# Kernel optimization log

Hardware: AMD Instinct MI355X
Metric: run time of the kernel (lower is better)

Reference implementation:

```python
import jax, jax.numpy as jnp
import numpy as np

TOP_K = 2  # num_experts_per_tok


def setup_inputs() -> dict:
    key = jax.random.key(0)
    k1, k2, k3, k4, k5 = jax.random.split(key, 5)
    T, H, F, E = 2048, 2048, 1024, 8
    hidden_states = jax.random.normal(k1, (T, H), dtype=jnp.float32)
    router_logits = jax.random.normal(k2, (T, E), dtype=jnp.float32)
    s = 1.0 / np.sqrt(H)
    w1 = jax.random.normal(k3, (E, H, F), dtype=jnp.float32) * s  # gate proj
    w3 = jax.random.normal(k4, (E, H, F), dtype=jnp.float32) * s  # up proj
    w2 = jax.random.normal(k5, (E, F, H), dtype=jnp.float32) * (1.0 / np.sqrt(F))  # down proj
    return {"hidden_states": hidden_states, "router_logits": router_logits,
            "w1": w1, "w3": w3, "w2": w2}


def reference(hidden_states, router_logits, w1, w3, w2):
    # Top-K routing: softmax over raw logits, take top-k probs as combine weights
    # (renormalize_topk_logits=False, routed_scaling_factor=None).
    T, E = router_logits.shape
    probs = jax.nn.softmax(router_logits.astype(jnp.float32), axis=-1)  # (T, E)
    topk_w, topk_ids = jax.lax.top_k(probs, TOP_K)                      # (T, K)
    # Scatter combine weights into a dense (T, E) matrix (zeros off top-k).
    combine = jnp.zeros((T, E), dtype=probs.dtype).at[
        jnp.arange(T)[:, None], topk_ids].add(topk_w)                    # (T, E)

    x = hidden_states
    # SwiGLU expert FFN computed per-expert (dense over all tokens, masked by
    # combine weights -> same math as fused dispatch/grouped-GEMM/combine).
    g = jnp.einsum('th,ehf->etf', x, w1)          # (E, T, F) gate
    u = jnp.einsum('th,ehf->etf', x, w3)          # (E, T, F) up
    act = jax.nn.silu(g) * u                      # (E, T, F)
    act = act * combine.T[:, :, None]             # apply combine weight pre-down-proj
    y = jnp.einsum('etf,efh->th', act, w2)        # (T, H) combined over experts
    return y.astype(hidden_states.dtype)
```

## Files before the change

### kernel.cpp

```cpp
#include <hip/hip_runtime.h>
#include <stdint.h>

#define T_TOK 2048
#define HDIM  2048
#define FDIM  1024
#define NEXP  8

#define BM   128
#define BN   64
#define BK   64
#define NTHR 256
#define MT_MAX 16
#define NT1 (FDIM / BN)
#define NT2 (HDIM / BN)
#define NK1 (HDIM / BK)
#define NK2 (FDIM / BK)
#define GRID1 (NEXP * MT_MAX * NT1)
#define GRID2 (NEXP * MT_MAX * NT2)

typedef unsigned short u16;
typedef __attribute__((ext_vector_type(16))) float f32x16;
typedef __attribute__((ext_vector_type(8))) short bf16x8;

__device__ __forceinline__ u16 f2bf(float f) {
  uint32_t u = __float_as_uint(f);
  u += 0x7FFFu + ((u >> 16) & 1u);
  return (u16)(u >> 16);
}

__device__ __forceinline__ void glds16(const u16* src, u16* dst) {
  __builtin_amdgcn_global_load_lds(
      (const __attribute__((address_space(1))) uint32_t*)src,
      (__attribute__((address_space(3))) uint32_t*)dst, 16, 0, 0);
}

__global__ void route1_kernel(const float* __restrict__ logits,
                              int* __restrict__ tok_e, float* __restrict__ tok_w,
                              int* __restrict__ counts) {
  __shared__ int lcnt[NEXP];
  const int tid = threadIdx.x;
  const int t = blockIdx.x * 256 + tid;
  if (tid < NEXP) lcnt[tid] = 0;
  __syncthreads();
  float l[NEXP];
#pragma unroll
  for (int e = 0; e < NEXP; ++e) l[e] = logits[t * NEXP + e];
  float m = l[0];
#pragma unroll
  for (int e = 1; e < NEXP; ++e) m = fmaxf(m, l[e]);
  float p[NEXP]; float s = 0.f;
#pragma unroll
  for (int e = 0; e < NEXP; ++e) { p[e] = __expf(l[e] - m); s += p[e]; }
  float inv = 1.f / s;
  int i0 = 0; float p0 = p[0];
#pragma unroll
  for (int e = 1; e < NEXP; ++e) if (p[e] > p0) { p0 = p[e]; i0 = e; }
  int i1 = -1; float p1 = -1.f;
#pragma unroll
  for (int e = 0; e < NEXP; ++e) if (e != i0 && p[e] > p1) { p1 = p[e]; i1 = e; }
  tok_e[t] = i0 | (i1 << 8);
  tok_w[t * 2]     = p0 * inv;
  tok_w[t * 2 + 1] = p1 * inv;
  atomicAdd(&lcnt[i0], 1);
  atomicAdd(&lcnt[i1], 1);
  __syncthreads();
  if (tid < NEXP) atomicAdd(&counts[tid], lcnt[tid]);
}

__global__ void route2_kernel(const int* __restrict__ counts,
                              int* __restrict__ offsets, int* __restrict__ cursor) {
  if (threadIdx.x == 0) {
    int s = 0;
    for (int e = 0; e < NEXP; ++e) { offsets[e] = s; cursor[e] = s; s += counts[e]; }
    offsets[NEXP] = s;
  }
}

__global__ void route3_kernel(const int* __restrict__ tok_e, const float* __restrict__ tok_w,
                              int* __restrict__ cursor,
                              int* __restrict__ token_list, float* __restrict__ slot_w) {
  __shared__ int lcnt[NEXP], lbase[NEXP];
  const int tid = threadIdx.x;
  const int t = blockIdx.x * 256 + tid;
  if (tid < NEXP) lcnt[tid] = 0;
  __syncthreads();
  int ee = tok_e[t];
  int e0 = ee & 255, e1 = ee >> 8;
  int li0 = atomicAdd(&lcnt[e0], 1);
  int li1 = atomicAdd(&lcnt[e1], 1);
  __syncthreads();
  if (tid < NEXP) lbase[tid] = atomicAdd(&cursor[tid], lcnt[tid]);
  __syncthreads();
  int s0 = lbase[e0] + li0;
  int s1 = lbase[e1] + li1;
  token_list[s0] = t; slot_w[s0] = tok_w[t * 2];
  token_list[s1] = t; slot_w[s1] = tok_w[t * 2 + 1];
}

__global__ void convert_x_kernel(const float4* __restrict__ x, ushort4* __restrict__ xb) {
  int i = blockIdx.x * 256 + threadIdx.x;
  float4 v = x[i];
  ushort4 o;
  o.x = f2bf(v.x); o.y = f2bf(v.y); o.z = f2bf(v.z); o.w = f2bf(v.w);
  xb[i] = o;
}

__global__ __launch_bounds__(256)
void tconv_kernel(const float* __restrict__ src_, u16* __restrict__ dst_,
                  int R, int C) {
  const size_t msz = (size_t)R * C;
  const float* src = src_ + blockIdx.z * msz;
  u16* dst = dst_ + blockIdx.z * msz;
  const int r0 = blockIdx.y * 64;
  const int c0 = blockIdx.x * 64;
  __shared__ uint32_t T[64][33];
  const int t = threadIdx.x;
  {
    const int kp = t >> 3;
    const int cg = t & 7;
    const float* s0 = src + (size_t)(r0 + 2 * kp) * C + c0 + cg * 8;
    float4 a0 = *(const float4*)(s0);
    float4 a1 = *(const float4*)(s0 + 4);
    float4 b0 = *(const float4*)(s0 + C);
    float4 b1 = *(const float4*)(s0 + C + 4);
    T[cg * 8 + 0][kp] = (uint32_t)f2bf(a0.x) | ((uint32_t)f2bf(b0.x) << 16);
    T[cg * 8 + 1][kp] = (uint32_t)f2bf(a0.y) | ((uint32_t)f2bf(b0.y) << 16);
    T[cg * 8 + 2][kp] = (uint32_t)f2bf(a0.z) | ((uint32_t)f2bf(b0.z) << 16);
    T[cg * 8 + 3][kp] = (uint32_t)f2bf(a0.w) | ((uint32_t)f2bf(b0.w) << 16);
    T[cg * 8 + 4][kp] = (uint32_t)f2bf(a1.x) | ((uint32_t)f2bf(b1.x) << 16);
    T[cg * 8 + 5][kp] = (uint32_t)f2bf(a1.y) | ((uint32_t)f2bf(b1.y) << 16);
    T[cg * 8 + 6][kp] = (uint32_t)f2bf(a1.z) | ((uint32_t)f2bf(b1.z) << 16);
    T[cg * 8 + 7][kp] = (uint32_t)f2bf(a1.w) | ((uint32_t)f2bf(b1.w) << 16);
  }
  __syncthreads();
  {
    const int f = t >> 2;
    const int kg = t & 3;
    uint32_t v[8];
#pragma unroll
    for (int i = 0; i < 8; ++i) v[i] = T[f][kg * 8 + i];
    u16* d = dst + (size_t)(c0 + f) * R + r0 + kg * 16;
    uint4 w0 = {v[0], v[1], v[2], v[3]};
    uint4 w1 = {v[4], v[5], v[6], v[7]};
    *(uint4*)(d) = w0;
    *(uint4*)(d + 8) = w1;
  }
}

__global__ __launch_bounds__(NTHR, 3)
void gemm1_kernel(const u16* __restrict__ Xb,
                  const u16* __restrict__ w1t,
                  const u16* __restrict__ w3t,
                  const int* __restrict__ token_list,
                  const float* __restrict__ slot_w,
                  const int* __restrict__ counts,
                  const int* __restrict__ offsets,
                  u16* __restrict__ act) {
  const int bid = blockIdx.x;
  const int e  = bid >> 8;
  const int mt = (bid >> 4) & 15;
  const int nt = bid & 15;
  const int cnt = counts[e];
  if (mt * BM >= cnt) return;
  const int off = offsets[e];
  const int tid  = threadIdx.x;
  const int lane = tid & 63;
  const int wid  = tid >> 6;
  const int wr = wid >> 1;
  const int wc = wid & 1;

  __shared__ u16 A_lds[BM * BK];
  __shared__ u16 B1_lds[BN * BK];
  __shared__ u16 B3_lds[BN * BK];

  const u16* a_src[4];
#pragma unroll
  for (int i = 0; i < 4; ++i) {
    int row = (wid * 4 + i) * 8 + (lane >> 3);
    int mg = mt * BM + row;
    int mc = (mg < cnt) ? mg : (cnt - 1);
    int tok = token_list[off + mc];
    a_src[i] = Xb + (size_t)tok * HDIM + (((lane & 7) ^ (row & 7)) * 8);
  }
  const u16* b1_src[2];
  const u16* b3_src[2];
#pragma unroll
  for (int i = 0; i < 2; ++i) {
    int n = (wid * 2 + i) * 8 + (lane >> 3);
    size_t rowoff = ((size_t)e * FDIM + nt * BN + n) * HDIM + (((lane & 7) ^ (n & 7)) * 8);
    b1_src[i] = w1t + rowoff;
    b3_src[i] = w3t + rowoff;
  }

  f32x16 accg[2] = {};
  f32x16 accu[2] = {};

#pragma unroll
  for (int i = 0; i < 4; ++i) glds16(a_src[i], &A_lds[(wid * 4 + i) * 512]);
#pragma unroll
  for (int i = 0; i < 2; ++i) {
    glds16(b1_src[i], &B1_lds[(wid * 2 + i) * 512]);
    glds16(b3_src[i], &B3_lds[(wid * 2 + i) * 512]);
  }

#pragma unroll 1
  for (int t = 0; t < NK1; ++t) {
    __syncthreads();
    bf16x8 af[2][4], bg[4], bu[4];
#pragma unroll
    for (int m = 0; m < 2; ++m) {
      int R = wr * 64 + m * 32 + (lane & 31);
#pragma unroll
      for (int kk = 0; kk < 4; ++kk) {
        int gl = kk * 2 + (lane >> 5);
        af[m][kk] = *(const bf16x8*)&A_lds[R * BK + ((gl ^ (R & 7)) * 8)];
      }
    }
    {
      int R = wc * 32 + (lane & 31);
#pragma unroll
      for (int kk = 0; kk < 4; ++kk) {
        int gl = kk * 2 + (lane >> 5);
        int pos = R * BK + ((gl ^ (R & 7)) * 8);
        bg[kk] = *(const bf16x8*)&B1_lds[pos];
        bu[kk] = *(const bf16x8*)&B3_lds[pos];
      }
    }
    __syncthreads();
    if (t + 1 < NK1) {
      const int ks = (t + 1) * BK;
#pragma unroll
      for (int i = 0; i < 4; ++i) glds16(a_src[i] + ks, &A_lds[(wid * 4 + i) * 512]);
#pragma unroll
      for (int i = 0; i < 2; ++i) {
        glds16(b1_src[i] + ks, &B1_lds[(wid * 2 + i) * 512]);
        glds16(b3_src[i] + ks, &B3_lds[(wid * 2 + i) * 512]);
      }
    }
#pragma unroll
    for (int m = 0; m < 2; ++m)
#pragma unroll
      for (int kk = 0; kk < 4; ++kk) {
        accg[m] = __builtin_amdgcn_mfma_f32_32x32x16_bf16(af[m][kk], bg[kk], accg[m], 0, 0, 0);
        accu[m] = __builtin_amdgcn_mfma_f32_32x32x16_bf16(af[m][kk], bu[kk], accu[m], 0, 0, 0);
      }
  }

  const int fcol = nt * BN + wc * 32 + (lane & 31);
#pragma unroll
  for (int m = 0; m < 2; ++m) {
    int base = mt * BM + wr * 64 + m * 32 + 4 * (lane >> 5);
#pragma unroll
    for (int reg = 0; reg < 16; ++reg) {
      int mg = base + (reg & 3) + 8 * (reg >> 2);
      if (mg < cnt) {
        int slot = off + mg;
        float wgt = slot_w[slot];
        float g = accg[m][reg];
        float u = accu[m][reg];
        float sv = g / (1.f + __expf(-g));
        act[(size_t)slot * FDIM + fcol] = f2bf(sv * u * wgt);
      }
    }
  }
}

__global__ __launch_bounds__(NTHR, 4)
void gemm2_kernel(const u16* __restrict__ act,
                  const u16* __restrict__ w2t,
                  const int* __restrict__ token_list,
                  const int* __restrict__ counts,
                  const int* __restrict__ offsets,
                  float* __restrict__ y) {
  const int bid = blockIdx.x;
  const int e  = bid >> 9;
  const int mt = (bid >> 5) & 15;
  const int nt = bid & 31;
  const int cnt = counts[e];
  if (mt * BM >= cnt) return;
  const int off = offsets[e];
  const int tid  = threadIdx.x;
  const int lane = tid & 63;
  const int wid  = tid >> 6;
  const int wr = wid >> 1;
  const int wc = wid & 1;

  __shared__ u16 A_lds[BM * BK];
  __shared__ u16 B_lds[BN * BK];

  const u16* a_src[4];
#pragma unroll
  for (int i = 0; i < 4; ++i) {
    int row = (wid * 4 + i) * 8 + (lane >> 3);
    int mg = mt * BM + row;
    int mc = (mg < cnt) ? mg : (cnt - 1);
    a_src[i] = act + (size_t)(off + mc) * FDIM + (((lane & 7) ^ (row & 7)) * 8);
  }
  const u16* b_src[2];
#pragma unroll
  for (int i = 0; i < 2; ++i) {
    int n = (wid * 2 + i) * 8 + (lane >> 3);
    b_src[i] = w2t + ((size_t)e * HDIM + nt * BN + n) * FDIM + (((lane & 7) ^ (n & 7)) * 8);
  }

  f32x16 acc[2] = {};

#pragma unroll
  for (int i = 0; i < 4; ++i) glds16(a_src[i], &A_lds[(wid * 4 + i) * 512]);
#pragma unroll
  for (int i = 0; i < 2; ++i) glds16(b_src[i], &B_lds[(wid * 2 + i) * 512]);

#pragma unroll 1
  for (int t = 0; t < NK2; ++t) {
    __syncthreads();
    bf16x8 af[2][4], bb[4];
#pragma unroll
    for (int m = 0; m < 2; ++m) {
      int R = wr * 64 + m * 32 + (lane & 31);
#pragma unroll
      for (int kk = 0; kk < 4; ++kk) {
        int gl = kk * 2 + (lane >> 5);
        af[m][kk] = *(const bf16x8*)&A_lds[R * BK + ((gl ^ (R & 7)) * 8)];
      }
    }
    {
      int R = wc * 32 + (lane & 31);
#pragma unroll
      for (int kk = 0; kk < 4; ++kk) {
        int gl = kk * 2 + (lane >> 5);
        bb[kk] = *(const bf16x8*)&B_lds[R * BK + ((gl ^ (R & 7)) * 8)];
      }
    }
    __syncthreads();
    if (t + 1 < NK2) {
      const int ks = (t + 1) * BK;
#pragma unroll
      for (int i = 0; i < 4; ++i) glds16(a_src[i] + ks, &A_lds[(wid * 4 + i) * 512]);
#pragma unroll
      for (int i = 0; i < 2; ++i) glds16(b_src[i] + ks, &B_lds[(wid * 2 + i) * 512]);
    }
#pragma unroll
    for (int m = 0; m < 2; ++m)
#pragma unroll
      for (int kk = 0; kk < 4; ++kk)
        acc[m] = __builtin_amdgcn_mfma_f32_32x32x16_bf16(af[m][kk], bb[kk], acc[m], 0, 0, 0);
  }

  const int hcol = nt * BN + wc * 32 + (lane & 31);
#pragma unroll
  for (int m = 0; m < 2; ++m) {
    int base = mt * BM + wr * 64 + m * 32 + 4 * (lane >> 5);
#pragma unroll
    for (int reg = 0; reg < 16; ++reg) {
      int mg = base + (reg & 3) + 8 * (reg >> 2);
      if (mg < cnt) {
        int slot = off + mg;
        int tok = token_list[slot];
        unsafeAtomicAdd(y + (size_t)tok * HDIM + hcol, acc[m][reg]);
      }
    }
  }
}

extern "C" void kernel_launch(void* const* d_in, const int* in_sizes, int n_in,
                              void* d_out, int out_size, void* d_ws, size_t ws_size,
                              hipStream_t stream) {
  (void)in_sizes; (void)n_in; (void)out_size; (void)ws_size;
  const float* hs     = (const float*)d_in[0];
  const float* logits = (const float*)d_in[1];
  const float* w1     = (const float*)d_in[2];
  const float* w3     = (const float*)d_in[3];
  const float* w2     = (const float*)d_in[4];
  float* y = (float*)d_out;

  uint8_t* ws = (uint8_t*)d_ws;
  int*   token_list = (int*)(ws);
  float* slot_w     = (float*)(ws + (16 << 10));
  int*   counts     = (int*)(ws + (32 << 10));
  int*   offsets    = (int*)(ws + (32 << 10) + 128);
  int*   cursor     = (int*)(ws + (32 << 10) + 256);
  int*   tok_e      = (int*)(ws + (33 << 10));
  float* tok_w      = (float*)(ws + (42 << 10));
  const size_t MB = 1 << 20;
  u16*   Xb  = (u16*)(ws + (64 << 10));
  u16*   act = (u16*)(ws + (64 << 10) + 8 * MB);
  u16*   w1t = (u16*)(ws + (64 << 10) + 16 * MB);
  u16*   w3t = (u16*)(ws + (64 << 10) + 48 * MB);
  u16*   w2t = (u16*)(ws + (64 << 10) + 80 * MB);

  hipMemsetAsync(counts, 0, NEXP * sizeof(int), stream);
  route1_kernel<<<T_TOK / 256, 256, 0, stream>>>(logits, tok_e, tok_w, counts);
  route2_kernel<<<1, 64, 0, stream>>>(counts, offsets, cursor);
  route3_kernel<<<T_TOK / 256, 256, 0, stream>>>(tok_e, tok_w, cursor, token_list, slot_w);
  convert_x_kernel<<<(T_TOK * HDIM / 4) / 256, 256, 0, stream>>>((const float4*)hs, (ushort4*)Xb);
  tconv_kernel<<<dim3(FDIM / 64, HDIM / 64, NEXP), 256, 0, stream>>>(w1, w1t, HDIM, FDIM);
  tconv_kernel<<<dim3(FDIM / 64, HDIM / 64, NEXP), 256, 0, stream>>>(w3, w3t, HDIM, FDIM);
  tconv_kernel<<<dim3(HDIM / 64, FDIM / 64, NEXP), 256, 0, stream>>>(w2, w2t, FDIM, HDIM);
  hipMemsetAsync(d_out, 0, (size_t)T_TOK * HDIM * sizeof(float), stream);
  gemm1_kernel<<<GRID1, NTHR, 0, stream>>>(Xb, w1t, w3t, token_list, slot_w, counts, offsets, act);
  gemm2_kernel<<<GRID2, NTHR, 0, stream>>>(act, w2t, token_list, counts, offsets, y);
}
```

Measured before the change: 196.5 us.

## Double-buffer LDS in both GEMMs and merge weight transpose launches

Both expert GEMMs now use two LDS buffers, so the next K-tile's global-to-LDS loads are issued at the top of each iteration and the second barrier per iteration goes away. MFMA blocks are wrapped in s_setprio to favour the math waves. Launch bounds drop by one wave per SIMD to fit the doubled shared memory. The three weight transpose/convert launches are merged into one 3D-grid kernel, where blocks outside the matrix early-exit, to cut launch overhead.

```diff
diff --git a/kernel.cpp b/kernel.cpp
--- a/kernel.cpp
+++ b/kernel.cpp
@@ -106,11 +106,20 @@
 }
 
 __global__ __launch_bounds__(256)
-void tconv_kernel(const float* __restrict__ src_, u16* __restrict__ dst_,
-                  int R, int C) {
-  const size_t msz = (size_t)R * C;
-  const float* src = src_ + blockIdx.z * msz;
-  u16* dst = dst_ + blockIdx.z * msz;
+void tconv_all_kernel(const float* __restrict__ w1, const float* __restrict__ w3,
+                      const float* __restrict__ w2,
+                      u16* __restrict__ w1t, u16* __restrict__ w3t, u16* __restrict__ w2t) {
+  const int z = blockIdx.z;
+  const int which = z >> 3;
+  const int e = z & 7;
+  const float* src; u16* dst; int R, C;
+  if (which == 0)      { src = w1; dst = w1t; R = HDIM; C = FDIM; }
+  else if (which == 1) { src = w3; dst = w3t; R = HDIM; C = FDIM; }
+  else                 { src = w2; dst = w2t; R = FDIM; C = HDIM; }
+  if (blockIdx.x * 64 >= (unsigned)C || blockIdx.y * 64 >= (unsigned)R) return;
+  const size_t msz = (size_t)HDIM * FDIM;
+  src += (size_t)e * msz;
+  dst += (size_t)e * msz;
   const int r0 = blockIdx.y * 64;
   const int c0 = blockIdx.x * 64;
   __shared__ uint32_t T[64][33];
@@ -140,14 +149,14 @@
 #pragma unroll
     for (int i = 0; i < 8; ++i) v[i] = T[f][kg * 8 + i];
     u16* d = dst + (size_t)(c0 + f) * R + r0 + kg * 16;
-    uint4 w0 = {v[0], v[1], v[2], v[3]};
-    uint4 w1 = {v[4], v[5], v[6], v[7]};
-    *(uint4*)(d) = w0;
-    *(uint4*)(d + 8) = w1;
-  }
-}
-
-__global__ __launch_bounds__(NTHR, 3)
+    uint4 q0 = {v[0], v[1], v[2], v[3]};
+    uint4 q1 = {v[4], v[5], v[6], v[7]};
+    *(uint4*)(d) = q0;
+    *(uint4*)(d + 8) = q1;
+  }
+}
+
+__global__ __launch_bounds__(NTHR, 2)
 void gemm1_kernel(const u16* __restrict__ Xb,
                   const u16* __restrict__ w1t,
                   const u16* __restrict__ w3t,
@@ -169,9 +178,9 @@
   const int wr = wid >> 1;
   const int wc = wid & 1;
 
-  __shared__ u16 A_lds[BM * BK];
-  __shared__ u16 B1_lds[BN * BK];
-  __shared__ u16 B3_lds[BN * BK];
+  __shared__ u16 A_lds[2][BM * BK];
+  __shared__ u16 B1_lds[2][BN * BK];
+  __shared__ u16 B3_lds[2][BN * BK];
 
   const u16* a_src[4];
 #pragma unroll
@@ -196,16 +205,28 @@
   f32x16 accu[2] = {};
 
 #pragma unroll
-  for (int i = 0; i < 4; ++i) glds16(a_src[i], &A_lds[(wid * 4 + i) * 512]);
+  for (int i = 0; i < 4; ++i) glds16(a_src[i], &A_lds[0][(wid * 4 + i) * 512]);
 #pragma unroll
   for (int i = 0; i < 2; ++i) {
-    glds16(b1_src[i], &B1_lds[(wid * 2 + i) * 512]);
-    glds16(b3_src[i], &B3_lds[(wid * 2 + i) * 512]);
+    glds16(b1_src[i], &B1_lds[0][(wid * 2 + i) * 512]);
+    glds16(b3_src[i], &B3_lds[0][(wid * 2 + i) * 512]);
   }
 
 #pragma unroll 1
   for (int t = 0; t < NK1; ++t) {
     __syncthreads();
+    const int cur = t & 1;
+    if (t + 1 < NK1) {
+      const int ks = (t + 1) * BK;
+      const int nb = cur ^ 1;
+#pragma unroll
+      for (int i = 0; i < 4; ++i) glds16(a_src[i] + ks, &A_lds[nb][(wid * 4 + i) * 512]);
+#pragma unroll
+      for (int i = 0; i < 2; ++i) {
+        glds16(b1_src[i] + ks, &B1_lds[nb][(wid * 2 + i) * 512]);
+        glds16(b3_src[i] + ks, &B3_lds[nb][(wid * 2 + i) * 512]);
+      }
+    }
     bf16x8 af[2][4], bg[4], bu[4];
 #pragma unroll
     for (int m = 0; m < 2; ++m) {
@@ -213,7 +234,7 @@
 #pragma unroll
       for (int kk = 0; kk < 4; ++kk) {
         int gl = kk * 2 + (lane >> 5);
-        af[m][kk] = *(const bf16x8*)&A_lds[R * BK + ((gl ^ (R & 7)) * 8)];
+        af[m][kk] = *(const bf16x8*)&A_lds[cur][R * BK + ((gl ^ (R & 7)) * 8)];
       }
     }
     {
@@ -222,21 +243,11 @@
       for (int kk = 0; kk < 4; ++kk) {
         int gl = kk * 2 + (lane >> 5);
         int pos = R * BK + ((gl ^ (R & 7)) * 8);
-        bg[kk] = *(const bf16x8*)&B1_lds[pos];
-        bu[kk] = *(const bf16x8*)&B3_lds[pos];
-      }
-    }
-    __syncthreads();
-    if (t + 1 < NK1) {
-      const int ks = (t + 1) * BK;
-#pragma unroll
-      for (int i = 0; i < 4; ++i) glds16(a_src[i] + ks, &A_lds[(wid * 4 + i) * 512]);
-#pragma unroll
-      for (int i = 0; i < 2; ++i) {
-        glds16(b1_src[i] + ks, &B1_lds[(wid * 2 + i) * 512]);
-        glds16(b3_src[i] + ks, &B3_lds[(wid * 2 + i) * 512]);
-      }
-    }
+        bg[kk] = *(const bf16x8*)&B1_lds[cur][pos];
+        bu[kk] = *(const bf16x8*)&B3_lds[cur][pos];
+      }
+    }
+    __builtin_amdgcn_s_setprio(1);
 #pragma unroll
     for (int m = 0; m < 2; ++m)
 #pragma unroll
@@ -244,6 +255,7 @@
         accg[m] = __builtin_amdgcn_mfma_f32_32x32x16_bf16(af[m][kk], bg[kk], accg[m], 0, 0, 0);
         accu[m] = __builtin_amdgcn_mfma_f32_32x32x16_bf16(af[m][kk], bu[kk], accu[m], 0, 0, 0);
       }
+    __builtin_amdgcn_s_setprio(0);
   }
 
   const int fcol = nt * BN + wc * 32 + (lane & 31);
@@ -265,7 +277,7 @@
   }
 }
 
-__global__ __launch_bounds__(NTHR, 4)
+__global__ __launch_bounds__(NTHR, 3)
 void gemm2_kernel(const u16* __restrict__ act,
                   const u16* __restrict__ w2t,
                   const int* __restrict__ token_list,
@@ -285,8 +297,8 @@
   const int wr = wid >> 1;
   const int wc = wid & 1;
 
-  __shared__ u16 A_lds[BM * BK];
-  __shared__ u16 B_lds[BN * BK];
+  __shared__ u16 A_lds[2][BM * BK];
+  __shared__ u16 B_lds[2][BN * BK];
 
   const u16* a_src[4];
 #pragma unroll
@@ -306,13 +318,22 @@
   f32x16 acc[2] = {};
 
 #pragma unroll
-  for (int i = 0; i < 4; ++i) glds16(a_src[i], &A_lds[(wid * 4 + i) * 512]);
-#pragma unroll
-  for (int i = 0; i < 2; ++i) glds16(b_src[i], &B_lds[(wid * 2 + i) * 512]);
+  for (int i = 0; i < 4; ++i) glds16(a_src[i], &A_lds[0][(wid * 4 + i) * 512]);
+#pragma unroll
+  for (int i = 0; i < 2; ++i) glds16(b_src[i], &B_lds[0][(wid * 2 + i) * 512]);
 
 #pragma unroll 1
   for (int t = 0; t < NK2; ++t) {
     __syncthreads();
+    const int cur = t & 1;
+    if (t + 1 < NK2) {
+      const int ks = (t + 1) * BK;
+      const int nb = cur ^ 1;
+#pragma unroll
+      for (int i = 0; i < 4; ++i) glds16(a_src[i] + ks, &A_lds[nb][(wid * 4 + i) * 512]);
+#pragma unroll
+      for (int i = 0; i < 2; ++i) glds16(b_src[i] + ks, &B_lds[nb][(wid * 2 + i) * 512]);
+    }
     bf16x8 af[2][4], bb[4];
 #pragma unroll
     for (int m = 0; m < 2; ++m) {
@@ -320,7 +341,7 @@
 #pragma unroll
       for (int kk = 0; kk < 4; ++kk) {
         int gl = kk * 2 + (lane >> 5);
-        af[m][kk] = *(const bf16x8*)&A_lds[R * BK + ((gl ^ (R & 7)) * 8)];
+        af[m][kk] = *(const bf16x8*)&A_lds[cur][R * BK + ((gl ^ (R & 7)) * 8)];
       }
     }
     {
@@ -328,22 +349,16 @@
 #pragma unroll
       for (int kk = 0; kk < 4; ++kk) {
         int gl = kk * 2 + (lane >> 5);
-        bb[kk] = *(const bf16x8*)&B_lds[R * BK + ((gl ^ (R & 7)) * 8)];
-      }
-    }
-    __syncthreads();
-    if (t + 1 < NK2) {
-      const int ks = (t + 1) * BK;
-#pragma unroll
-      for (int i = 0; i < 4; ++i) glds16(a_src[i] + ks, &A_lds[(wid * 4 + i) * 512]);
-#pragma unroll
-      for (int i = 0; i < 2; ++i) glds16(b_src[i] + ks, &B_lds[(wid * 2 + i) * 512]);
-    }
+        bb[kk] = *(const bf16x8*)&B_lds[cur][R * BK + ((gl ^ (R & 7)) * 8)];
+      }
+    }
+    __builtin_amdgcn_s_setprio(1);
 #pragma unroll
     for (int m = 0; m < 2; ++m)
 #pragma unroll
       for (int kk = 0; kk < 4; ++kk)
         acc[m] = __builtin_amdgcn_mfma_f32_32x32x16_bf16(af[m][kk], bb[kk], acc[m], 0, 0, 0);
+    __builtin_amdgcn_s_setprio(0);
   }
 
   const int hcol = nt * BN + wc * 32 + (lane & 31);
@@ -393,9 +408,7 @@
   route2_kernel<<<1, 64, 0, stream>>>(counts, offsets, cursor);
   route3_kernel<<<T_TOK / 256, 256, 0, stream>>>(tok_e, tok_w, cursor, token_list, slot_w);
   convert_x_kernel<<<(T_TOK * HDIM / 4) / 256, 256, 0, stream>>>((const float4*)hs, (ushort4*)Xb);
-  tconv_kernel<<<dim3(FDIM / 64, HDIM / 64, NEXP), 256, 0, stream>>>(w1, w1t, HDIM, FDIM);
-  tconv_kernel<<<dim3(FDIM / 64, HDIM / 64, NEXP), 256, 0, stream>>>(w3, w3t, HDIM, FDIM);
-  tconv_kernel<<<dim3(HDIM / 64, FDIM / 64, NEXP), 256, 0, stream>>>(w2, w2t, FDIM, HDIM);
+  tconv_all_kernel<<<dim3(32, 32, 24), 256, 0, stream>>>(w1, w3, w2, w1t, w3t, w2t);
   hipMemsetAsync(d_out, 0, (size_t)T_TOK * HDIM * sizeof(float), stream);
   gemm1_kernel<<<GRID1, NTHR, 0, stream>>>(Xb, w1t, w3t, token_list, slot_w, counts, offsets, act);
   gemm2_kernel<<<GRID2, NTHR, 0, stream>>>(act, w2t, token_list, counts, offsets, y);
```

After: 242.7 us. +23.5%, slower.

## Fuse weight fp32-to-bf16 transpose into GEMM B-tile loading

Applied to the files above, without the earlier changes.

Drops the separate tconv passes over w1, w3 and w2. Instead, each GEMM block loads fp32 weight rows into registers, converts and transposes them into a padded LDS tile, and prefetches the next k-slice while computing. This removes a full write and read of bf16 weight copies. In exchange it re-reads fp32 weights per M tile and adds conversion ALU work and register pressure in the main loop. It also adds s_setprio around the MFMA blocks and lowers gemm2's occupancy hint.

```diff
diff --git a/kernel.cpp b/kernel.cpp
--- a/kernel.cpp
+++ b/kernel.cpp
@@ -7,16 +7,18 @@
 #define NEXP  8
 
 #define BM   128
-#define BN   64
 #define BK   64
 #define NTHR 256
 #define MT_MAX 16
-#define NT1 (FDIM / BN)
-#define NT2 (HDIM / BN)
+#define BN1  64
+#define BN2  64
+#define NT1 (FDIM / BN1)
+#define NT2 (HDIM / BN2)
 #define NK1 (HDIM / BK)
 #define NK2 (FDIM / BK)
 #define GRID1 (NEXP * MT_MAX * NT1)
 #define GRID2 (NEXP * MT_MAX * NT2)
+#define BSTRIDE 34
 
 typedef unsigned short u16;
 typedef __attribute__((ext_vector_type(16))) float f32x16;
@@ -28,10 +30,22 @@
   return (u16)(u >> 16);
 }
 
+__device__ __forceinline__ uint32_t pack2(float lo, float hi) {
+  return (uint32_t)f2bf(lo) | ((uint32_t)f2bf(hi) << 16);
+}
+
 __device__ __forceinline__ void glds16(const u16* src, u16* dst) {
   __builtin_amdgcn_global_load_lds(
       (const __attribute__((address_space(1))) uint32_t*)src,
       (__attribute__((address_space(3))) uint32_t*)dst, 16, 0, 0);
+}
+
+__device__ __forceinline__ bf16x8 bfrag(const uint32_t* base) {
+  uint2 q0 = *(const uint2*)(base);
+  uint2 q1 = *(const uint2*)(base + 2);
+  union { uint4 u; bf16x8 b; } cv;
+  cv.u = make_uint4(q0.x, q0.y, q1.x, q1.y);
+  return cv.b;
 }
 
 __global__ void route1_kernel(const float* __restrict__ logits,
@@ -105,52 +119,10 @@
   xb[i] = o;
 }
 
-__global__ __launch_bounds__(256)
-void tconv_kernel(const float* __restrict__ src_, u16* __restrict__ dst_,
-                  int R, int C) {
-  const size_t msz = (size_t)R * C;
-  const float* src = src_ + blockIdx.z * msz;
-  u16* dst = dst_ + blockIdx.z * msz;
-  const int r0 = blockIdx.y * 64;
-  const int c0 = blockIdx.x * 64;
-  __shared__ uint32_t T[64][33];
-  const int t = threadIdx.x;
-  {
-    const int kp = t >> 3;
-    const int cg = t & 7;
-    const float* s0 = src + (size_t)(r0 + 2 * kp) * C + c0 + cg * 8;
-    float4 a0 = *(const float4*)(s0);
-    float4 a1 = *(const float4*)(s0 + 4);
-    float4 b0 = *(const float4*)(s0 + C);
-    float4 b1 = *(const float4*)(s0 + C + 4);
-    T[cg * 8 + 0][kp] = (uint32_t)f2bf(a0.x) | ((uint32_t)f2bf(b0.x) << 16);
-    T[cg * 8 + 1][kp] = (uint32_t)f2bf(a0.y) | ((uint32_t)f2bf(b0.y) << 16);
-    T[cg * 8 + 2][kp] = (uint32_t)f2bf(a0.z) | ((uint32_t)f2bf(b0.z) << 16);
-    T[cg * 8 + 3][kp] = (uint32_t)f2bf(a0.w) | ((uint32_t)f2bf(b0.w) << 16);
-    T[cg * 8 + 4][kp] = (uint32_t)f2bf(a1.x) | ((uint32_t)f2bf(b1.x) << 16);
-    T[cg * 8 + 5][kp] = (uint32_t)f2bf(a1.y) | ((uint32_t)f2bf(b1.y) << 16);
-    T[cg * 8 + 6][kp] = (uint32_t)f2bf(a1.z) | ((uint32_t)f2bf(b1.z) << 16);
-    T[cg * 8 + 7][kp] = (uint32_t)f2bf(a1.w) | ((uint32_t)f2bf(b1.w) << 16);
-  }
-  __syncthreads();
-  {
-    const int f = t >> 2;
-    const int kg = t & 3;
-    uint32_t v[8];
-#pragma unroll
-    for (int i = 0; i < 8; ++i) v[i] = T[f][kg * 8 + i];
-    u16* d = dst + (size_t)(c0 + f) * R + r0 + kg * 16;
-    uint4 w0 = {v[0], v[1], v[2], v[3]};
-    uint4 w1 = {v[4], v[5], v[6], v[7]};
-    *(uint4*)(d) = w0;
-    *(uint4*)(d + 8) = w1;
-  }
-}
-
 __global__ __launch_bounds__(NTHR, 3)
 void gemm1_kernel(const u16* __restrict__ Xb,
-                  const u16* __restrict__ w1t,
-                  const u16* __restrict__ w3t,
+                  const float* __restrict__ w1,
+                  const float* __restrict__ w3,
                   const int* __restrict__ token_list,
                   const float* __restrict__ slot_w,
                   const int* __restrict__ counts,
@@ -170,8 +142,8 @@
   const int wc = wid & 1;
 
   __shared__ u16 A_lds[BM * BK];
-  __shared__ u16 B1_lds[BN * BK];
-  __shared__ u16 B3_lds[BN * BK];
+  __shared__ uint32_t B1u[BN1 * BSTRIDE];
+  __shared__ uint32_t B3u[BN1 * BSTRIDE];
 
   const u16* a_src[4];
 #pragma unroll
@@ -182,30 +154,53 @@
     int tok = token_list[off + mc];
     a_src[i] = Xb + (size_t)tok * HDIM + (((lane & 7) ^ (row & 7)) * 8);
   }
-  const u16* b1_src[2];
-  const u16* b3_src[2];
-#pragma unroll
-  for (int i = 0; i < 2; ++i) {
-    int n = (wid * 2 + i) * 8 + (lane >> 3);
-    size_t rowoff = ((size_t)e * FDIM + nt * BN + n) * HDIM + (((lane & 7) ^ (n & 7)) * 8);
-    b1_src[i] = w1t + rowoff;
-    b3_src[i] = w3t + rowoff;
-  }
+
+  const int kp = tid >> 3;
+  const int cg = tid & 7;
+  const float* p1 = w1 + (size_t)e * HDIM * FDIM + (size_t)(2 * kp) * FDIM + nt * BN1 + cg * 8;
+  const float* p3 = w3 + (size_t)e * HDIM * FDIM + (size_t)(2 * kp) * FDIM + nt * BN1 + cg * 8;
 
   f32x16 accg[2] = {};
   f32x16 accu[2] = {};
 
+  float4 x1a, x1b, x1c, x1d, x3a, x3b, x3c, x3d;
+#define LOADB(ks)                                                      \
+  { const float* q1 = p1 + (size_t)(ks) * FDIM;                        \
+    const float* q3 = p3 + (size_t)(ks) * FDIM;                        \
+    x1a = *(const float4*)(q1);        x1b = *(const float4*)(q1 + 4); \
+    x1c = *(const float4*)(q1 + FDIM); x1d = *(const float4*)(q1 + FDIM + 4); \
+    x3a = *(const float4*)(q3);        x3b = *(const float4*)(q3 + 4); \
+    x3c = *(const float4*)(q3 + FDIM); x3d = *(const float4*)(q3 + FDIM + 4); }
+
 #pragma unroll
   for (int i = 0; i < 4; ++i) glds16(a_src[i], &A_lds[(wid * 4 + i) * 512]);
-#pragma unroll
-  for (int i = 0; i < 2; ++i) {
-    glds16(b1_src[i], &B1_lds[(wid * 2 + i) * 512]);
-    glds16(b3_src[i], &B3_lds[(wid * 2 + i) * 512]);
-  }
+  LOADB(0);
 
 #pragma unroll 1
   for (int t = 0; t < NK1; ++t) {
+    {
+      uint32_t* d1 = &B1u[(cg * 8) * BSTRIDE + kp];
+      uint32_t* d3 = &B3u[(cg * 8) * BSTRIDE + kp];
+      d1[0 * BSTRIDE] = pack2(x1a.x, x1c.x);
+      d1[1 * BSTRIDE] = pack2(x1a.y, x1c.y);
+      d1[2 * BSTRIDE] = pack2(x1a.z, x1c.z);
+      d1[3 * BSTRIDE] = pack2(x1a.w, x1c.w);
+      d1[4 * BSTRIDE] = pack2(x1b.x, x1d.x);
+      d1[5 * BSTRIDE] = pack2(x1b.y, x1d.y);
+      d1[6 * BSTRIDE] = pack2(x1b.z, x1d.z);
+      d1[7 * BSTRIDE] = pack2(x1b.w, x1d.w);
+      d3[0 * BSTRIDE] = pack2(x3a.x, x3c.x);
+      d3[1 * BSTRIDE] = pack2(x3a.y, x3c.y);
+      d3[2 * BSTRIDE] = pack2(x3a.z, x3c.z);
+      d3[3 * BSTRIDE] = pack2(x3a.w, x3c.w);
+      d3[4 * BSTRIDE] = pack2(x3b.x, x3d.x);
+      d3[5 * BSTRIDE] = pack2(x3b.y, x3d.y);
+      d3[6 * BSTRIDE] = pack2(x3b.z, x3d.z);
+      d3[7 * BSTRIDE] = pack2(x3b.w, x3d.w);
+    }
     __syncthreads();
+    if (t + 1 < NK1) LOADB((t + 1) * BK);
+
     bf16x8 af[2][4], bg[4], bu[4];
 #pragma unroll
     for (int m = 0; m < 2; ++m) {
@@ -217,13 +212,13 @@
       }
     }
     {
-      int R = wc * 32 + (lane & 31);
+      int n = wc * 32 + (lane & 31);
+      const uint32_t* b1p = &B1u[n * BSTRIDE + (lane >> 5) * 4];
+      const uint32_t* b3p = &B3u[n * BSTRIDE + (lane >> 5) * 4];
 #pragma unroll
       for (int kk = 0; kk < 4; ++kk) {
-        int gl = kk * 2 + (lane >> 5);
-        int pos = R * BK + ((gl ^ (R & 7)) * 8);
-        bg[kk] = *(const bf16x8*)&B1_lds[pos];
-        bu[kk] = *(const bf16x8*)&B3_lds[pos];
+        bg[kk] = bfrag(b1p + kk * 8);
+        bu[kk] = bfrag(b3p + kk * 8);
       }
     }
     __syncthreads();
@@ -231,12 +226,8 @@
       const int ks = (t + 1) * BK;
 #pragma unroll
       for (int i = 0; i < 4; ++i) glds16(a_src[i] + ks, &A_lds[(wid * 4 + i) * 512]);
-#pragma unroll
-      for (int i = 0; i < 2; ++i) {
-        glds16(b1_src[i] + ks, &B1_lds[(wid * 2 + i) * 512]);
-        glds16(b3_src[i] + ks, &B3_lds[(wid * 2 + i) * 512]);
-      }
-    }
+    }
+    __builtin_amdgcn_s_setprio(1);
 #pragma unroll
     for (int m = 0; m < 2; ++m)
 #pragma unroll
@@ -244,9 +235,11 @@
         accg[m] = __builtin_amdgcn_mfma_f32_32x32x16_bf16(af[m][kk], bg[kk], accg[m], 0, 0, 0);
         accu[m] = __builtin_amdgcn_mfma_f32_32x32x16_bf16(af[m][kk], bu[kk], accu[m], 0, 0, 0);
       }
-  }
-
-  const int fcol = nt * BN + wc * 32 + (lane & 31);
+    __builtin_amdgcn_s_setprio(0);
+  }
+#undef LOADB
+
+  const int fcol = nt * BN1 + wc * 32 + (lane & 31);
 #pragma unroll
   for (int m = 0; m < 2; ++m) {
     int base = mt * BM + wr * 64 + m * 32 + 4 * (lane >> 5);
@@ -265,9 +258,9 @@
   }
 }
 
-__global__ __launch_bounds__(NTHR, 4)
+__global__ __launch_bounds__(NTHR, 3)
 void gemm2_kernel(const u16* __restrict__ act,
-                  const u16* __restrict__ w2t,
+                  const float* __restrict__ w2,
                   const int* __restrict__ token_list,
                   const int* __restrict__ counts,
                   const int* __restrict__ offsets,
@@ -286,7 +279,7 @@
   const int wc = wid & 1;
 
   __shared__ u16 A_lds[BM * BK];
-  __shared__ u16 B_lds[BN * BK];
+  __shared__ uint32_t Bu[BN2 * BSTRIDE];
 
   const u16* a_src[4];
 #pragma unroll
@@ -296,23 +289,38 @@
     int mc = (mg < cnt) ? mg : (cnt - 1);
     a_src[i] = act + (size_t)(off + mc) * FDIM + (((lane & 7) ^ (row & 7)) * 8);
   }
-  const u16* b_src[2];
-#pragma unroll
-  for (int i = 0; i < 2; ++i) {
-    int n = (wid * 2 + i) * 8 + (lane >> 3);
-    b_src[i] = w2t + ((size_t)e * HDIM + nt * BN + n) * FDIM + (((lane & 7) ^ (n & 7)) * 8);
-  }
+  const int kp = tid >> 3;
+  const int cg = tid & 7;
+  const float* p2 = w2 + (size_t)e * FDIM * HDIM + (size_t)(2 * kp) * HDIM + nt * BN2 + cg * 8;
 
   f32x16 acc[2] = {};
 
+  float4 xa, xb, xc, xd;
+#define LOADB2(ks)                                                     \
+  { const float* q = p2 + (size_t)(ks) * HDIM;                         \
+    xa = *(const float4*)(q);        xb = *(const float4*)(q + 4);     \
+    xc = *(const float4*)(q + HDIM); xd = *(const float4*)(q + HDIM + 4); }
+
 #pragma unroll
   for (int i = 0; i < 4; ++i) glds16(a_src[i], &A_lds[(wid * 4 + i) * 512]);
-#pragma unroll
-  for (int i = 0; i < 2; ++i) glds16(b_src[i], &B_lds[(wid * 2 + i) * 512]);
+  LOADB2(0);
 
 #pragma unroll 1
   for (int t = 0; t < NK2; ++t) {
+    {
+      uint32_t* d = &Bu[(cg * 8) * BSTRIDE + kp];
+      d[0 * BSTRIDE] = pack2(xa.x, xc.x);
+      d[1 * BSTRIDE] = pack2(xa.y, xc.y);
+      d[2 * BSTRIDE] = pack2(xa.z, xc.z);
+      d[3 * BSTRIDE] = pack2(xa.w, xc.w);
+      d[4 * BSTRIDE] = pack2(xb.x, xd.x);
+      d[5 * BSTRIDE] = pack2(xb.y, xd.y);
+      d[6 * BSTRIDE] = pack2(xb.z, xd.z);
+      d[7 * BSTRIDE] = pack2(xb.w, xd.w);
+    }
     __syncthreads();
+    if (t + 1 < NK2) LOADB2((t + 1) * BK);
+
     bf16x8 af[2][4], bb[4];
 #pragma unroll
     for (int m = 0; m < 2; ++m) {
@@ -324,29 +332,28 @@
       }
     }
     {
-      int R = wc * 32 + (lane & 31);
-#pragma unroll
-      for (int kk = 0; kk < 4; ++kk) {
-        int gl = kk * 2 + (lane >> 5);
-        bb[kk] = *(const bf16x8*)&B_lds[R * BK + ((gl ^ (R & 7)) * 8)];
-      }
+      int n = wc * 32 + (lane & 31);
+      const uint32_t* bp = &Bu[n * BSTRIDE + (lane >> 5) * 4];
+#pragma unroll
+      for (int kk = 0; kk < 4; ++kk) bb[kk] = bfrag(bp + kk * 8);
     }
     __syncthreads();
     if (t + 1 < NK2) {
       const int ks = (t + 1) * BK;
 #pragma unroll
       for (int i = 0; i < 4; ++i) glds16(a_src[i] + ks, &A_lds[(wid * 4 + i) * 512]);
-#pragma unroll
-      for (int i = 0; i < 2; ++i) glds16(b_src[i] + ks, &B_lds[(wid * 2 + i) * 512]);
-    }
+    }
+    __builtin_amdgcn_s_setprio(1);
 #pragma unroll
     for (int m = 0; m < 2; ++m)
 #pragma unroll
       for (int kk = 0; kk < 4; ++kk)
         acc[m] = __builtin_amdgcn_mfma_f32_32x32x16_bf16(af[m][kk], bb[kk], acc[m], 0, 0, 0);
-  }
-
-  const int hcol = nt * BN + wc * 32 + (lane & 31);
+    __builtin_amdgcn_s_setprio(0);
+  }
+#undef LOADB2
+
+  const int hcol = nt * BN2 + wc * 32 + (lane & 31);
 #pragma unroll
   for (int m = 0; m < 2; ++m) {
     int base = mt * BM + wr * 64 + m * 32 + 4 * (lane >> 5);
@@ -384,19 +391,13 @@
   const size_t MB = 1 << 20;
   u16*   Xb  = (u16*)(ws + (64 << 10));
   u16*   act = (u16*)(ws + (64 << 10) + 8 * MB);
-  u16*   w1t = (u16*)(ws + (64 << 10) + 16 * MB);
-  u16*   w3t = (u16*)(ws + (64 << 10) + 48 * MB);
-  u16*   w2t = (u16*)(ws + (64 << 10) + 80 * MB);
 
   hipMemsetAsync(counts, 0, NEXP * sizeof(int), stream);
   route1_kernel<<<T_TOK / 256, 256, 0, stream>>>(logits, tok_e, tok_w, counts);
   route2_kernel<<<1, 64, 0, stream>>>(counts, offsets, cursor);
   route3_kernel<<<T_TOK / 256, 256, 0, stream>>>(tok_e, tok_w, cursor, token_list, slot_w);
   convert_x_kernel<<<(T_TOK * HDIM / 4) / 256, 256, 0, stream>>>((const float4*)hs, (ushort4*)Xb);
-  tconv_kernel<<<dim3(FDIM / 64, HDIM / 64, NEXP), 256, 0, stream>>>(w1, w1t, HDIM, FDIM);
-  tconv_kernel<<<dim3(FDIM / 64, HDIM / 64, NEXP), 256, 0, stream>>>(w3, w3t, HDIM, FDIM);
-  tconv_kernel<<<dim3(HDIM / 64, FDIM / 64, NEXP), 256, 0, stream>>>(w2, w2t, FDIM, HDIM);
   hipMemsetAsync(d_out, 0, (size_t)T_TOK * HDIM * sizeof(float), stream);
-  gemm1_kernel<<<GRID1, NTHR, 0, stream>>>(Xb, w1t, w3t, token_list, slot_w, counts, offsets, act);
-  gemm2_kernel<<<GRID2, NTHR, 0, stream>>>(act, w2t, token_list, counts, offsets, y);
-}
+  gemm1_kernel<<<GRID1, NTHR, 0, stream>>>(Xb, w1, w3, token_list, slot_w, counts, offsets, act);
+  gemm2_kernel<<<GRID2, NTHR, 0, stream>>>(act, w2, token_list, counts, offsets, y);
+}
```

Result: slower. 341.4 us (+73.7%).
